# Optimization experiments

Hardware: AMD Instinct MI355X
Metric: run time of the kernel (lower is better)

The kernel has to match this reference:

```python
import jax, jax.numpy as jnp
import numpy as np

B, L, E, P, LABEL, NLAYERS, NSTATE = 32, 1024, 512, 336, 48, 3, 32  # NSTATE = d_state//2 (conjugate-pair diagonal S4D)


def setup_inputs() -> dict:
    key = jax.random.key(0)
    ks = jax.random.split(key, 10)
    H, N = E, NSTATE
    x_enc = jax.random.normal(ks[0], (B, L, E), jnp.float32)
    x_mark_enc = jax.random.normal(ks[1], (B, L, 4), jnp.float32)
    x_dec_true = jax.random.normal(ks[2], (B, LABEL + P, E), jnp.float32)
    x_mark_dec = jax.random.normal(ks[3], (B, LABEL + P, 4), jnp.float32)
    # S4D parameters, stacked over layers. S4D-Lin init: A = -1/2 + i*pi*n
    log_dt = (jax.random.uniform(ks[4], (NLAYERS, H), jnp.float32)
              * (np.log(0.1) - np.log(0.001)) + np.log(0.001))
    A_re = -0.5 * jnp.ones((NLAYERS, H, N), jnp.float32)
    A_im = jnp.tile(np.pi * jnp.arange(N, dtype=np.float32), (NLAYERS, H, 1))
    C_re = jax.random.normal(ks[5], (NLAYERS, H, N), jnp.float32) * (0.5 ** 0.5)
    C_im = jax.random.normal(ks[6], (NLAYERS, H, N), jnp.float32) * (0.5 ** 0.5)
    Dskip = jax.random.normal(ks[7], (NLAYERS, H), jnp.float32)
    Wo = jax.random.normal(ks[8], (NLAYERS, 2 * H, H), jnp.float32) / np.sqrt(H)
    bo = jnp.zeros((NLAYERS, 2 * H), jnp.float32)
    W_out = jax.random.normal(ks[9], (P, L), jnp.float32) / np.sqrt(L)
    b_out = jnp.zeros((P,), jnp.float32)
    return dict(x_enc=x_enc, x_mark_enc=x_mark_enc, x_dec_true=x_dec_true,
                x_mark_dec=x_mark_dec, log_dt=log_dt, A_re=A_re, A_im=A_im,
                C_re=C_re, C_im=C_im, Dskip=Dskip, Wo=Wo, bo=bo,
                W_out=W_out, b_out=b_out)


def s4_layer(u, log_dt, A_re, A_im, C_re, C_im, Dskip, Wo, bo):
    """u: (B, H, L). Diagonal S4 (S4D) layer: SSM kernel -> FFT conv -> D skip -> GELU -> GLU linear."""
    H, N = A_re.shape
    Ln = u.shape[-1]
    dt = jnp.exp(log_dt)[:, None]                       # (H,1)
    A = A_re + 1j * A_im                                # (H,N)
    dtA = dt * A                                        # (H,N)
    # ZOH discretization of B=1: dB = (exp(dt*A)-1)/A
    Ct = (C_re + 1j * C_im) * (jnp.expm1(dtA) / A)      # (H,N)
    # Vandermonde: K[h,l] = 2*Re( sum_n Ct[h,n] * exp(dtA[h,n])^l )
    vand = jnp.exp(dtA[:, :, None] * jnp.arange(Ln, dtype=jnp.float32))  # (H,N,L) complex
    K = 2.0 * jnp.einsum('hn,hnl->hl', Ct, vand).real   # (H,L)
    # Causal convolution via FFT with zero padding to 2L
    k_f = jnp.fft.rfft(K, n=2 * Ln)                     # (H, L+1)
    u_f = jnp.fft.rfft(u, n=2 * Ln)                     # (B, H, L+1)
    y = jnp.fft.irfft(u_f * k_f, n=2 * Ln)[..., :Ln]    # (B, H, L)
    y = y + u * Dskip[:, None]
    y = jax.nn.gelu(y)
    z = jnp.einsum('oh,bhl->bol', Wo, y) + bo[None, :, None]  # (B, 2H, L)
    return z[:, :H] * jax.nn.sigmoid(z[:, H:])          # GLU over channels


def reference(x_enc, x_mark_enc, x_dec_true, x_mark_dec, log_dt, A_re, A_im,
              C_re, C_im, Dskip, Wo, bo, W_out, b_out):
    x = jnp.transpose(x_enc, (0, 2, 1))                 # (B, E, L)
    for i in range(NLAYERS):
        x = s4_layer(x, log_dt[i], A_re[i], A_im[i], C_re[i], C_im[i],
                     Dskip[i], Wo[i], bo[i])
    # output Linear over the time axis: (B, E, L) -> (B, E, P), then permute
    x_dec = jnp.einsum('ps,bhs->bhp', W_out, x) + b_out[None, None, :]
    return jnp.transpose(x_dec, (0, 2, 1))              # (B, P, E)
```

## Files before the change

kernel.cpp:

```cpp
#include <hip/hip_runtime.h>
#include <math.h>

typedef _Float16 f16;
typedef f16 f16x4 __attribute__((ext_vector_type(4)));
typedef f16 f16x8 __attribute__((ext_vector_type(8)));
typedef float f32x4 __attribute__((ext_vector_type(4)));

namespace {

constexpr int kB  = 32;
constexpr int kL  = 1024;
constexpr int kH  = 512;
constexpr int kP  = 336;
constexpr int kNL = 3;
constexpr int kNS = 32;
constexpr int kM  = 16;

__device__ __forceinline__ void llds16(const void* g, void* s) {
  __builtin_amdgcn_global_load_lds((const __attribute__((address_space(1))) void*)g,
                                   (__attribute__((address_space(3))) void*)s, 16, 0, 0);
}

__device__ __forceinline__ float gelu_tanh(float y0) {
  float x3 = y0 * y0 * y0;
  float a = 0.7978845608028654f * fmaf(0.044715f, x3, y0);
  float aa = fminf(a, 15.f);
  float ex = __expf(2.f * aa);
  float th = 1.f - 2.f / (ex + 1.f);
  return 0.5f * y0 * (1.f + th);
}

template <int DIST>
__device__ __forceinline__ float dpp_shr0(float x) {
  return __builtin_bit_cast(float,
      __builtin_amdgcn_update_dpp(0, __builtin_bit_cast(int, x),
                                  0x110 | DIST, 0xF, 0xF, true));
}

__device__ __forceinline__ void csq(float& r, float& i) {
  float nr = r * r - i * i;
  i = 2.f * r * i;
  r = nr;
}

template <int DIST, int NCT>
__device__ __forceinline__ void scan_level(f32x4 (&a)[NCT], float t0r, float t0i,
                                           float t1r, float t1i) {
#pragma unroll
  for (int ct = 0; ct < NCT; ct++) {
    float r0 = dpp_shr0<DIST>(a[ct][0]);
    float i0 = dpp_shr0<DIST>(a[ct][1]);
    float r1 = dpp_shr0<DIST>(a[ct][2]);
    float i1 = dpp_shr0<DIST>(a[ct][3]);
    a[ct][0] = fmaf(t0r, r0, fmaf(-t0i, i0, a[ct][0]));
    a[ct][1] = fmaf(t0r, i0, fmaf(t0i, r0, a[ct][1]));
    a[ct][2] = fmaf(t1r, r1, fmaf(-t1i, i1, a[ct][2]));
    a[ct][3] = fmaf(t1r, i1, fmaf(t1i, r1, a[ct][3]));
  }
}

__global__ __launch_bounds__(64) void prep_kernel(
    const float* __restrict__ log_dt, const float* __restrict__ A_re,
    const float* __restrict__ A_im, const float* __restrict__ C_re,
    const float* __restrict__ C_im, const float* __restrict__ Dskip,
    f16* __restrict__ Afrag_c, f16* __restrict__ Afrag_a,
    float* __restrict__ rT) {
  int lh = blockIdx.x;
  int tid = threadIdx.x;
  __shared__ float pr[32][65], pi[32][65];
  __shared__ float cre_s[32], cim_s[32];
  __shared__ float kt[64];

  float dt = expf(log_dt[lh]);
  if (tid < 32) {
    int n = tid;
    int idx = lh * 32 + n;
    float ar = A_re[idx], ai = A_im[idx];
    float dr = dt * ar, di = dt * ai;
    float er = expf(dr), cd = cosf(di), sd = sinf(di);
    float rr = er * cd, ri = er * sd;
    float sh = sinf(0.5f * di);
    float mr = expm1f(dr) * cd - 2.f * sh * sh;
    float mi = ri;
    float inv = 1.f / (ar * ar + ai * ai);
    float qr = (mr * ar + mi * ai) * inv;
    float qi = (mi * ar - mr * ai) * inv;
    float cre = C_re[idx], cim = C_im[idx];
    cre_s[n] = 2.f * (cre * qr - cim * qi);
    cim_s[n] = 2.f * (cre * qi + cim * qr);
    float xr = 1.f, xi = 0.f;
    for (int k = 0; k < 65; k++) {
      pr[n][k] = xr;
      pi[n][k] = xi;
      float nxr = xr * rr - xi * ri;
      float nxi = xr * ri + xi * rr;
      xr = nxr;
      xi = nxi;
    }
    rT[idx * 2] = pr[n][64];
    rT[idx * 2 + 1] = pi[n][64];
  }
  __syncthreads();
  {
    int d = tid;
    float s = 0.f;
    for (int n = 0; n < 32; n++) s += cre_s[n] * pr[n][d] - cim_s[n] * pi[n][d];
    if (d == 0) s += Dskip[lh];
    kt[d] = s;
  }
  __syncthreads();
  f16* ac = Afrag_c + (size_t)lh * 8192;
#pragma unroll
  for (int it = 0; it < 16; it++) {
    int ks = it >> 2, rt = it & 3;
    int t = rt * 16 + (tid & 15);
    int kbase = ks * 32 + (tid >> 4) * 8;
    f16x8 v;
#pragma unroll
    for (int j = 0; j < 8; j++) {
      int k = kbase + j;
      float val;
      if (k < 64) {
        val = (t >= k) ? kt[t - k] : 0.f;
      } else {
        int s2 = k - 64;
        int n = s2 >> 1;
        float prr = pr[n][t + 1], pii = pi[n][t + 1];
        val = ((s2 & 1) == 0) ? (cre_s[n] * prr - cim_s[n] * pii)
                              : -(cre_s[n] * pii + cim_s[n] * prr);
      }
      v[j] = (f16)val;
    }
    *(f16x8*)(ac + (size_t)(it * 64 + tid) * 8) = v;
  }
  f16* aa = Afrag_a + (size_t)lh * 4096;
#pragma unroll
  for (int it = 0; it < 8; it++) {
    int ks = it >> 2, rt = it & 3;
    int s2 = rt * 16 + (tid & 15);
    int n = s2 >> 1;
    int kbase = ks * 32 + (tid >> 4) * 8;
    f16x8 v;
#pragma unroll
    for (int j = 0; j < 8; j++) {
      int t = kbase + j;
      v[j] = (f16)(((s2 & 1) == 0) ? pr[n][63 - t] : pi[n][63 - t]);
    }
    *(f16x8*)(aa + (size_t)(it * 64 + tid) * 8) = v;
  }
}

__global__ void f32_to_f16_kernel(const float* __restrict__ s, f16* __restrict__ d,
                                  int n) {
  int i = blockIdx.x * 256 + threadIdx.x;
  if (i < n) d[i] = (f16)s[i];
}

__global__ __launch_bounds__(256) void wo_frag_kernel(const float* __restrict__ Wo,
                                                      f16* __restrict__ woF) {
  int layer = blockIdx.y, mt = blockIdx.x;
  int t = threadIdx.x;
  int lane = t & 63;
  const float* w = Wo + (size_t)layer * 2 * kH * kH;
  f16* dst = woF + ((size_t)layer * 64 + mt) * 8192;
  int row = mt * 16 + (lane & 15);
  int cbase = (lane >> 4) * 8;
#pragma unroll
  for (int it = 0; it < 4; it++) {
    int ks = it * 4 + (t >> 6);
    f16x8 v;
#pragma unroll
    for (int j = 0; j < 8; j++) v[j] = (f16)w[(size_t)row * kH + ks * 32 + cbase + j];
    *(f16x8*)(dst + (size_t)(ks * 64 + lane) * 8) = v;
  }
}

__global__ __launch_bounds__(256) void transpose_kernel(const float* __restrict__ x,
                                                        f16* __restrict__ u) {
  __shared__ float tile[32][33];
  int b = blockIdx.z;
  int l0 = blockIdx.x * 32, e0 = blockIdx.y * 32;
  int tx = threadIdx.x, ty = threadIdx.y;
#pragma unroll
  for (int k = 0; k < 4; k++)
    tile[ty + 8 * k][tx] = x[((size_t)b * kL + (size_t)(l0 + ty + 8 * k)) * kH + e0 + tx];
  __syncthreads();
#pragma unroll
  for (int k = 0; k < 4; k++)
    u[((size_t)b * kH + (size_t)(e0 + ty + 8 * k)) * kL + l0 + tx] =
        (f16)tile[tx][ty + 8 * k];
}

__global__ __launch_bounds__(256) void t16f_kernel(const f16* __restrict__ y,
                                                   f16* __restrict__ ytF) {
  __shared__ f16 tile[64][72];
  int b = blockIdx.z;
  int h0 = blockIdx.y * 64, l0 = blockIdx.x * 64;
  int t = threadIdx.x;
  int row = t >> 3, lc = t & 7;
#pragma unroll
  for (int r2 = 0; r2 < 2; r2++) {
    int r = row + 32 * r2;
    *(f16x8*)&tile[r][lc * 8] =
        *(const f16x8*)(y + (size_t)(b * kH + h0 + r) * kL + l0 + lc * 8);
  }
  __syncthreads();
  int li = t >> 2, sc = t & 3;
#pragma unroll
  for (int s2 = 0; s2 < 2; s2++) {
    int s = sc + 4 * s2;
    f16x8 v;
#pragma unroll
    for (int j = 0; j < 8; j++) v[j] = tile[s * 8 + j][li];
    size_t off = ((((size_t)b * 64 + (l0 >> 4) + (li >> 4)) * 16) + (h0 >> 5) + s2) * 512
                 + (size_t)(sc * 16 + (li & 15)) * 8;
    *(f16x8*)(ytF + off) = v;
  }
}

__global__ __launch_bounds__(64) void chunk_wy_kernel(
    const f16* __restrict__ u, const f16* __restrict__ Afrag_a,
    const f16* __restrict__ Afrag_c, const float* __restrict__ rT,
    f16* __restrict__ yout, int layer) {
  __shared__ __align__(16) f16 Sl[2][16][72];
  int h = blockIdx.y;
  int lane = threadIdx.x;
  int col0 = blockIdx.x * 32;
  const f16* aa = Afrag_a + (size_t)(layer * kH + h) * 4096;
  const f16* ac = Afrag_c + (size_t)(layer * kH + h) * 8192;
  int k8 = lane >> 4, cl = lane & 15;

  const f16* gu[2];
#pragma unroll
  for (int ct = 0; ct < 2; ct++) {
    int col = col0 + ct * 16 + cl;
    int b = col >> 4, c = col & 15;
    gu[ct] = u + (size_t)(b * kH + h) * kL + c * 64 + k8 * 8;
  }

  f32x4 acc[4][2] = {};
#pragma unroll
  for (int ks = 0; ks < 2; ks++) {
    f16x8 af[4], ufl[2];
#pragma unroll
    for (int rt = 0; rt < 4; rt++)
      af[rt] = *(const f16x8*)(aa + (size_t)((ks * 4 + rt) * 64 + lane) * 8);
#pragma unroll
    for (int ct = 0; ct < 2; ct++)
      ufl[ct] = *(const f16x8*)(gu[ct] + ks * 32);
#pragma unroll
    for (int rt = 0; rt < 4; rt++)
#pragma unroll
      for (int ct = 0; ct < 2; ct++)
        acc[rt][ct] =
            __builtin_amdgcn_mfma_f32_16x16x32_f16(af[rt], ufl[ct], acc[rt][ct], 0, 0, 0);
  }

  int lhb = (layer * kH + h) * 32;
#pragma unroll
  for (int rt = 0; rt < 4; rt++) {
    int n0 = rt * 8 + k8 * 2;
    float t0r = rT[(lhb + n0) * 2], t0i = rT[(lhb + n0) * 2 + 1];
    float t1r = rT[(lhb + n0 + 1) * 2], t1i = rT[(lhb + n0 + 1) * 2 + 1];
    scan_level<1, 2>(acc[rt], t0r, t0i, t1r, t1i);
    csq(t0r, t0i); csq(t1r, t1i);
    scan_level<2, 2>(acc[rt], t0r, t0i, t1r, t1i);
    csq(t0r, t0i); csq(t1r, t1i);
    scan_level<4, 2>(acc[rt], t0r, t0i, t1r, t1i);
    csq(t0r, t0i); csq(t1r, t1i);
    scan_level<8, 2>(acc[rt], t0r, t0i, t1r, t1i);
  }

#pragma unroll
  for (int rt = 0; rt < 4; rt++)
#pragma unroll
    for (int ct = 0; ct < 2; ct++) {
      f16x4 v;
#pragma unroll
      for (int reg = 0; reg < 4; reg++) {
        v[reg] = (f16)dpp_shr0<1>(acc[rt][ct][reg]);
      }
      *(f16x4*)&Sl[ct][cl][rt * 16 + k8 * 4] = v;
    }
  asm volatile("s_waitcnt lgkmcnt(0)" ::: "memory");

  f32x4 accD[4][2] = {};
#pragma unroll
  for (int ks = 0; ks < 4; ks++) {
    f16x8 af[4], bf[2];
#pragma unroll
    for (int rt = 0; rt < 4; rt++)
      af[rt] = *(const f16x8*)(ac + (size_t)((ks * 4 + rt) * 64 + lane) * 8);
#pragma unroll
    for (int ct = 0; ct < 2; ct++) {
      if (ks < 2)
        bf[ct] = *(const f16x8*)(gu[ct] + ks * 32);
      else
        bf[ct] = *(const f16x8*)&Sl[ct][cl][(ks - 2) * 32 + k8 * 8];
    }
#pragma unroll
    for (int rt = 0; rt < 4; rt++)
#pragma unroll
      for (int ct = 0; ct < 2; ct++)
        accD[rt][ct] =
            __builtin_amdgcn_mfma_f32_16x16x32_f16(af[rt], bf[ct], accD[rt][ct], 0, 0, 0);
  }

#pragma unroll
  for (int ct = 0; ct < 2; ct++) {
    int col = col0 + ct * 16 + cl;
    int b = col >> 4, c = col & 15;
    f16* yp = yout + (size_t)(b * kH + h) * kL + c * 64;
#pragma unroll
    for (int rt = 0; rt < 4; rt++) {
      f16x4 v;
#pragma unroll
      for (int reg = 0; reg < 4; reg++) v[reg] = (f16)gelu_tanh(accD[rt][ct][reg]);
      *(f16x4*)(yp + rt * 16 + k8 * 4) = v;
    }
  }
}

__global__ __launch_bounds__(256) void glu_mfma_kernel(
    const f16* __restrict__ ytF,
    const f16* __restrict__ woF,
    const float* __restrict__ bo,
    f16* __restrict__ uout) {
  int tid = threadIdx.x;
  int lane = tid & 63, w = tid >> 6;
  int wm = w >> 1, wn = w & 1;
  int b = blockIdx.z, h0 = blockIdx.y * 64, l0 = blockIdx.x * 128;

  const f16* gB[4];
#pragma unroll
  for (int nt = 0; nt < 4; ++nt)
    gB[nt] = ytF + ((size_t)(b * 64 + (l0 >> 4) + wn * 4 + nt) * 16) * 512 +
             (size_t)lane * 8;

  const f16* gA[4];
#pragma unroll
  for (int i = 0; i < 4; ++i) {
    int mt = (i < 2) ? ((h0 >> 4) + wm * 2 + i) : (32 + (h0 >> 4) + wm * 2 + (i - 2));
    gA[i] = woF + ((size_t)mt * 16 * 64 + lane) * 8;
  }

  f32x4 acc[4][4] = {};
  f16x8 bv[2][4];

#pragma unroll
  for (int nt = 0; nt < 4; ++nt) bv[0][nt] = *(const f16x8*)(gB[nt]);

#pragma unroll
  for (int kc = 0; kc < 16; ++kc) {
    int cur = kc & 1, nxt = cur ^ 1;
    if (kc < 15) {
#pragma unroll
      for (int nt = 0; nt < 4; ++nt)
        bv[nxt][nt] = *(const f16x8*)(gB[nt] + (size_t)(kc + 1) * 512);
    }
    f16x8 av[4];
#pragma unroll
    for (int i = 0; i < 4; ++i)
      av[i] = *(const f16x8*)(gA[i] + (size_t)kc * 512);
#pragma unroll
    for (int i = 0; i < 4; ++i)
#pragma unroll
      for (int nt = 0; nt < 4; ++nt)
        acc[i][nt] =
            __builtin_amdgcn_mfma_f32_16x16x32_f16(av[i], bv[cur][nt], acc[i][nt], 0, 0, 0);
  }

  int col = lane & 15, q = lane >> 4;
  f16* ub = uout + (size_t)b * kH * kL;
#pragma unroll
  for (int i = 0; i < 2; ++i) {
#pragma unroll
    for (int reg = 0; reg < 4; ++reg) {
      int h = h0 + wm * 32 + i * 16 + q * 4 + reg;
      float b1 = bo[h], b2 = bo[h + kH];
#pragma unroll
      for (int nt = 0; nt < 4; ++nt) {
        float z1 = acc[i][nt][reg] + b1;
        float z2 = acc[i + 2][nt][reg] + b2;
        float sg = 1.f / (1.f + __expf(-z2));
        ub[(size_t)h * kL + l0 + wn * 64 + nt * 16 + col] = (f16)(z1 * sg);
      }
    }
  }
}

__global__ __launch_bounds__(256) void final_mfma_kernel(
    const f16* __restrict__ x, const f16* __restrict__ wout,
    const float* __restrict__ bout, float* __restrict__ outp) {
  __shared__ __align__(16) f16 At[16][64][8];
  __shared__ __align__(16) f16 Bt[16][64][8];
  int tid = threadIdx.x;
  int lane = tid & 63, w = tid >> 6;
  int wm = w >> 1, wn = w & 1;
  int lr = lane & 15, lc = lane >> 4;
  int b = blockIdx.z, p0 = blockIdx.y * 128, h0 = blockIdx.x * 128;
  const f16* xb = x + (size_t)b * kH * kL;

  f32x4 acc[4][4] = {};

  const f16* gA[4];
  const f16* gB[4];
#pragma unroll
  for (int i = 0; i < 4; ++i) {
    int st = w * 4 + i, mt = st >> 1, ks = st & 1;
    int prow = p0 + mt * 16 + lr;
    if (prow > kP - 1) prow = kP - 1;
    gA[i] = wout + (size_t)prow * kL + ks * 32 + lc * 8;
    int hrow = h0 + mt * 16 + lr;
    gB[i] = xb + (size_t)hrow * kL + ks * 32 + lc * 8;
  }

  for (int k0 = 0; k0 < kL; k0 += 64) {
#pragma unroll
    for (int i = 0; i < 4; ++i) {
      int st = w * 4 + i;
      llds16(gA[i] + k0, &At[st][0][0]);
      llds16(gB[i] + k0, &Bt[st][0][0]);
    }
    __syncthreads();
#pragma unroll
    for (int ks = 0; ks < 2; ++ks) {
      f16x8 av[4], bv[4];
#pragma unroll
      for (int i = 0; i < 4; ++i)
        av[i] = *(const f16x8*)At[(wm * 4 + i) * 2 + ks][lane];
#pragma unroll
      for (int nt = 0; nt < 4; ++nt)
        bv[nt] = *(const f16x8*)Bt[(wn * 4 + nt) * 2 + ks][lane];
#pragma unroll
      for (int i = 0; i < 4; ++i)
#pragma unroll
        for (int nt = 0; nt < 4; ++nt)
          acc[i][nt] =
              __builtin_amdgcn_mfma_f32_16x16x32_f16(av[i], bv[nt], acc[i][nt], 0, 0, 0);
    }
    __syncthreads();
  }

  int col = lane & 15, q = lane >> 4;
  float* ob = outp + (size_t)b * kP * kH;
#pragma unroll
  for (int i = 0; i < 4; ++i) {
#pragma unroll
    for (int reg = 0; reg < 4; ++reg) {
      int p = p0 + wm * 64 + i * 16 + q * 4 + reg;
      if (p < kP) {
        float bv2 = bout[p];
#pragma unroll
        for (int nt = 0; nt < 4; ++nt)
          ob[(size_t)p * kH + h0 + wn * 64 + nt * 16 + col] = acc[i][nt][reg] + bv2;
      }
    }
  }
}

}

extern "C" void kernel_launch(void* const* d_in, const int* in_sizes, int n_in,
                              void* d_out, int out_size, void* d_ws, size_t ws_size,
                              hipStream_t stream) {
  const float* x_enc  = (const float*)d_in[0];
  const float* log_dt = (const float*)d_in[4];
  const float* A_re   = (const float*)d_in[5];
  const float* A_im   = (const float*)d_in[6];
  const float* C_re   = (const float*)d_in[7];
  const float* C_im   = (const float*)d_in[8];
  const float* Dskip  = (const float*)d_in[9];
  const float* Wo     = (const float*)d_in[10];
  const float* bo     = (const float*)d_in[11];
  const float* W_out  = (const float*)d_in[12];
  const float* b_out  = (const float*)d_in[13];
  float* out = (float*)d_out;

  char* wsb = (char*)d_ws;
  f16* u16    = (f16*)(wsb);
  f16* ybuf   = (f16*)(wsb + 33554432);
  f16* ytF    = (f16*)(wsb + 67108864);
  f16* woF    = (f16*)(wsb + 100663296);
  f16* wout16 = (f16*)(wsb + 103809024);
  f16* afc    = (f16*)(wsb + 104497152);
  f16* afa    = (f16*)(wsb + 129662976);
  float* rT   = (float*)(wsb + 142245888);

  const int nwp = kP * kL;
  f32_to_f16_kernel<<<(nwp + 255) / 256, 256, 0, stream>>>(W_out, wout16, nwp);
  wo_frag_kernel<<<dim3(64, kNL), 256, 0, stream>>>(Wo, woF);

  prep_kernel<<<kNL * kH, 64, 0, stream>>>(log_dt, A_re, A_im, C_re, C_im, Dskip,
                                           afc, afa, rT);

  transpose_kernel<<<dim3(kL / 32, kH / 32, kB), dim3(32, 8), 0, stream>>>(x_enc, u16);

  for (int layer = 0; layer < kNL; layer++) {
    chunk_wy_kernel<<<dim3(16, kH), 64, 0, stream>>>(u16, afa, afc, rT, ybuf, layer);
    t16f_kernel<<<dim3(kL / 64, kH / 64, kB), 256, 0, stream>>>(ybuf, ytF);
    glu_mfma_kernel<<<dim3(kL / 128, kH / 64, kB), 256, 0, stream>>>(
        ytF, woF + (size_t)layer * 64 * 8192, bo + (size_t)layer * 2 * kH, u16);
  }

  final_mfma_kernel<<<dim3(kH / 128, 3, kB), 256, 0, stream>>>(u16, wout16, b_out, out);
}
```

Measured before the change: 476.7 us.

## Fuse fragment-layout transpose into chunked SSM kernel via shared-memory staging

Merges the separate t16f transpose kernel into the chunked scan kernel. Each block now runs 8 waves, one per channel, and stages the GELU outputs in shared memory so it can write them directly in the fragment layout the GLU MFMA kernel reads. This removes a full f16 write and re-read of the intermediate activation buffer plus one launch per layer. In exchange the block is larger, adds a __syncthreads, uses more LDS, and the per-element scalar LDS writes into Yt may cause bank conflicts.

```diff
diff --git a/kernel.cpp b/kernel.cpp
--- a/kernel.cpp
+++ b/kernel.cpp
@@ -191,40 +191,15 @@
         (f16)tile[tx][ty + 8 * k];
 }
 
-__global__ __launch_bounds__(256) void t16f_kernel(const f16* __restrict__ y,
-                                                   f16* __restrict__ ytF) {
-  __shared__ f16 tile[64][72];
-  int b = blockIdx.z;
-  int h0 = blockIdx.y * 64, l0 = blockIdx.x * 64;
-  int t = threadIdx.x;
-  int row = t >> 3, lc = t & 7;
-#pragma unroll
-  for (int r2 = 0; r2 < 2; r2++) {
-    int r = row + 32 * r2;
-    *(f16x8*)&tile[r][lc * 8] =
-        *(const f16x8*)(y + (size_t)(b * kH + h0 + r) * kL + l0 + lc * 8);
-  }
-  __syncthreads();
-  int li = t >> 2, sc = t & 3;
-#pragma unroll
-  for (int s2 = 0; s2 < 2; s2++) {
-    int s = sc + 4 * s2;
-    f16x8 v;
-#pragma unroll
-    for (int j = 0; j < 8; j++) v[j] = tile[s * 8 + j][li];
-    size_t off = ((((size_t)b * 64 + (l0 >> 4) + (li >> 4)) * 16) + (h0 >> 5) + s2) * 512
-                 + (size_t)(sc * 16 + (li & 15)) * 8;
-    *(f16x8*)(ytF + off) = v;
-  }
-}
-
-__global__ __launch_bounds__(64) void chunk_wy_kernel(
+__global__ __launch_bounds__(512) void chunk_wyt_kernel(
     const f16* __restrict__ u, const f16* __restrict__ Afrag_a,
     const f16* __restrict__ Afrag_c, const float* __restrict__ rT,
-    f16* __restrict__ yout, int layer) {
-  __shared__ __align__(16) f16 Sl[2][16][72];
-  int h = blockIdx.y;
-  int lane = threadIdx.x;
+    f16* __restrict__ ytF, int layer) {
+  __shared__ __align__(16) f16 Sl[8][2][16][72];
+  __shared__ __align__(16) f16 Yt[32][65][8];
+  int tid = threadIdx.x;
+  int w = tid >> 6, lane = tid & 63;
+  int h = blockIdx.y * 8 + w;
   int col0 = blockIdx.x * 32;
   const f16* aa = Afrag_a + (size_t)(layer * kH + h) * 4096;
   const f16* ac = Afrag_c + (size_t)(layer * kH + h) * 8192;
@@ -280,7 +255,7 @@
       for (int reg = 0; reg < 4; reg++) {
         v[reg] = (f16)dpp_shr0<1>(acc[rt][ct][reg]);
       }
-      *(f16x4*)&Sl[ct][cl][rt * 16 + k8 * 4] = v;
+      *(f16x4*)&Sl[w][ct][cl][rt * 16 + k8 * 4] = v;
     }
   asm volatile("s_waitcnt lgkmcnt(0)" ::: "memory");
 
@@ -296,7 +271,7 @@
       if (ks < 2)
         bf[ct] = *(const f16x8*)(gu[ct] + ks * 32);
       else
-        bf[ct] = *(const f16x8*)&Sl[ct][cl][(ks - 2) * 32 + k8 * 8];
+        bf[ct] = *(const f16x8*)&Sl[w][ct][cl][(ks - 2) * 32 + k8 * 8];
     }
 #pragma unroll
     for (int rt = 0; rt < 4; rt++)
@@ -308,15 +283,28 @@
 
 #pragma unroll
   for (int ct = 0; ct < 2; ct++) {
-    int col = col0 + ct * 16 + cl;
+    int colIdx = ct * 16 + cl;
+#pragma unroll
+    for (int rt = 0; rt < 4; rt++) {
+#pragma unroll
+      for (int reg = 0; reg < 4; reg++) {
+        Yt[colIdx][rt * 16 + k8 * 4 + reg][w] = (f16)gelu_tanh(accD[rt][ct][reg]);
+      }
+    }
+  }
+  __syncthreads();
+
+  {
+    int colIdx = tid >> 4, pos = tid & 15;
+    int col = col0 + colIdx;
     int b = col >> 4, c = col & 15;
-    f16* yp = yout + (size_t)(b * kH + h) * kL + c * 64;
+    int kc = blockIdx.y >> 2, hi = blockIdx.y & 3;
 #pragma unroll
     for (int rt = 0; rt < 4; rt++) {
-      f16x4 v;
-#pragma unroll
-      for (int reg = 0; reg < 4; reg++) v[reg] = (f16)gelu_tanh(accD[rt][ct][reg]);
-      *(f16x4*)(yp + rt * 16 + k8 * 4) = v;
+      f16x8 word = *(const f16x8*)&Yt[colIdx][rt * 16 + pos][0];
+      size_t off = (((size_t)(b * 64 + c * 4 + rt) * 16) + kc) * 512 +
+                   (size_t)(hi * 16 + pos) * 8;
+      *(f16x8*)(ytF + off) = word;
     }
   }
 }
@@ -479,7 +467,6 @@
 
   char* wsb = (char*)d_ws;
   f16* u16    = (f16*)(wsb);
-  f16* ybuf   = (f16*)(wsb + 33554432);
   f16* ytF    = (f16*)(wsb + 67108864);
   f16* woF    = (f16*)(wsb + 100663296);
   f16* wout16 = (f16*)(wsb + 103809024);
@@ -497,8 +484,7 @@
   transpose_kernel<<<dim3(kL / 32, kH / 32, kB), dim3(32, 8), 0, stream>>>(x_enc, u16);
 
   for (int layer = 0; layer < kNL; layer++) {
-    chunk_wy_kernel<<<dim3(16, kH), 64, 0, stream>>>(u16, afa, afc, rT, ybuf, layer);
-    t16f_kernel<<<dim3(kL / 64, kH / 64, kB), 256, 0, stream>>>(ybuf, ytF);
+    chunk_wyt_kernel<<<dim3(16, kH / 8), 512, 0, stream>>>(u16, afa, afc, rT, ytF, layer);
     glu_mfma_kernel<<<dim3(kL / 128, kH / 64, kB), 256, 0, stream>>>(
         ytF, woF + (size_t)layer * 64 * 8192, bo + (size_t)layer * 2 * kH, u16);
   }
```

Result: faster. 439.9 us (-7.7%).
